# Kernel tuning notes

Hardware: AMD Instinct MI355X
Metric: run time of the kernel (lower is better)

The kernel has to match this reference:

```python
import jax, jax.numpy as jnp
import numpy as np

LN_EPS = 1e-5


def setup_inputs() -> dict:
    key = jax.random.key(0)
    ks = jax.random.split(key, 8)
    N, E, D = 50000, 800000, 128
    x = jax.random.normal(ks[0], (N, D), dtype=jnp.float32)
    edge_index = jax.random.randint(ks[1], (2, E), 0, N, dtype=jnp.int64)
    scale = 0.05
    return {
        "x": x,
        "edge_index": edge_index,
        "W1": jax.random.normal(ks[2], (2 * D, D), dtype=jnp.float32) * scale,
        "b1": jnp.zeros((D,), dtype=jnp.float32),
        "W2": jax.random.normal(ks[3], (D, D), dtype=jnp.float32) * scale,
        "b2": jnp.zeros((D,), dtype=jnp.float32),
        "W3": jax.random.normal(ks[4], (D, D), dtype=jnp.float32) * scale,
        "b3": jnp.zeros((D,), dtype=jnp.float32),
        "W4": jax.random.normal(ks[5], (D, D), dtype=jnp.float32) * scale,
        "b4": jnp.zeros((D,), dtype=jnp.float32),
        "gamma": jnp.ones((D,), dtype=jnp.float32),
        "beta": jnp.zeros((D,), dtype=jnp.float32),
    }


def _layernorm(h, gamma, beta):
    mu = jnp.mean(h, axis=-1, keepdims=True)
    var = jnp.mean(jnp.square(h - mu), axis=-1, keepdims=True)
    return (h - mu) * jax.lax.rsqrt(var + LN_EPS) * gamma + beta


def reference(x, edge_index, W1, b1, W2, b2, W3, b3, W4, b4, gamma, beta):
    num_nodes = x.shape[0]
    senders, receivers = edge_index[0], edge_index[1]
    # gather sender features [E, D], scatter-add to receivers -> [N, D]
    agg = jax.ops.segment_sum(x[senders], receivers, num_segments=num_nodes)
    h = jnp.concatenate([x, agg], axis=-1)  # [N, 2D]
    h = jax.nn.relu(h @ W1 + b1)
    h = jax.nn.relu(h @ W2 + b2)
    h = jax.nn.relu(h @ W3 + b3)
    h = h @ W4 + b4
    return _layernorm(h, gamma, beta)
```

## Files before the change

### kernel.cpp

```cpp
#include <hip/hip_runtime.h>
#include <hip/hip_bf16.h>

typedef short short8 __attribute__((ext_vector_type(8)));
typedef float f32x4 __attribute__((ext_vector_type(4)));

#define LN_EPS 1e-5f
#define NBLK 256

__device__ __forceinline__ unsigned short f2bf(float f) {
    unsigned int u = __builtin_bit_cast(unsigned int, f);
    unsigned int r = (u + 0x7FFFu + ((u >> 16) & 1u)) >> 16;
    return (unsigned short)r;
}
__device__ __forceinline__ float bf_lo(unsigned int v) {
    return __builtin_bit_cast(float, v << 16);
}
__device__ __forceinline__ float bf_hi(unsigned int v) {
    return __builtin_bit_cast(float, v & 0xFFFF0000u);
}

__device__ __forceinline__ bool edges_are_i64(const int* ei) {
    return ((ei[1] | ei[3] | ei[5] | ei[7]) == 0);
}

__device__ __forceinline__ void do_hist(
    const int* __restrict__ ei, int* __restrict__ BBC, int E, int chunk,
    int blk, int t, int* hist)
{
    hist[t] = 0;
    __syncthreads();
    int beg = blk * chunk;
    int end = min(E, beg + chunk);
    if (edges_are_i64(ei)) {
        const long long* e64 = (const long long*)ei;
        for (int e = beg + t; e < end; e += 256)
            atomicAdd(&hist[((int)e64[E + e]) >> 8], 1);
    } else {
        for (int e = beg + t; e < end; e += 256)
            atomicAdd(&hist[ei[E + e] >> 8], 1);
    }
    __syncthreads();
    BBC[t * NBLK + blk] = hist[t];
}

__device__ __forceinline__ void do_prep(
    const float* __restrict__ W1, const float* __restrict__ W2,
    const float* __restrict__ W3, const float* __restrict__ W4,
    unsigned short* __restrict__ wt1, unsigned short* __restrict__ wt2,
    unsigned short* __restrict__ wt3, unsigned short* __restrict__ wt4,
    const float4* __restrict__ x4, uint4* __restrict__ xb4, int total8,
    int idx)
{
    if (idx < 32768) {
        int k = idx >> 7, n = idx & 127;
        wt1[n * 256 + k] = f2bf(W1[idx]);
    } else if (idx < 49152) {
        int j = idx - 32768; int k = j >> 7, n = j & 127;
        wt2[n * 128 + k] = f2bf(W2[j]);
    } else if (idx < 65536) {
        int j = idx - 49152; int k = j >> 7, n = j & 127;
        wt3[n * 128 + k] = f2bf(W3[j]);
    } else if (idx < 81920) {
        int j = idx - 65536; int k = j >> 7, n = j & 127;
        wt4[n * 128 + k] = f2bf(W4[j]);
    } else {
        int i = idx - 81920;
        if (i < total8) {
            float4 a = x4[i * 2], b = x4[i * 2 + 1];
            uint4 o;
            o.x = (unsigned int)f2bf(a.x) | ((unsigned int)f2bf(a.y) << 16);
            o.y = (unsigned int)f2bf(a.z) | ((unsigned int)f2bf(a.w) << 16);
            o.z = (unsigned int)f2bf(b.x) | ((unsigned int)f2bf(b.y) << 16);
            o.w = (unsigned int)f2bf(b.z) | ((unsigned int)f2bf(b.w) << 16);
            xb4[i] = o;
        }
    }
}

__global__ __launch_bounds__(256) void hist_prep_kernel(
    const int* __restrict__ ei, int* __restrict__ BBC, int E, int chunk,
    const float* __restrict__ W1, const float* __restrict__ W2,
    const float* __restrict__ W3, const float* __restrict__ W4,
    unsigned short* __restrict__ wt1, unsigned short* __restrict__ wt2,
    unsigned short* __restrict__ wt3, unsigned short* __restrict__ wt4,
    const float4* __restrict__ x4, uint4* __restrict__ xb4, int total8)
{
    __shared__ int sh[256];
    int t = threadIdx.x;
    if (blockIdx.x < NBLK) {
        do_hist(ei, BBC, E, chunk, blockIdx.x, t, sh);
    } else {
        do_prep(W1, W2, W3, W4, wt1, wt2, wt3, wt4, x4, xb4, total8,
                (blockIdx.x - NBLK) * 256 + t);
    }
}

__global__ __launch_bounds__(256) void xcvt_kernel(
    const float4* __restrict__ x4, uint4* __restrict__ xb4, int total8)
{
    int i = blockIdx.x * 256 + threadIdx.x;
    if (i >= total8) return;
    float4 a = x4[i * 2], b = x4[i * 2 + 1];
    uint4 o;
    o.x = (unsigned int)f2bf(a.x) | ((unsigned int)f2bf(a.y) << 16);
    o.y = (unsigned int)f2bf(a.z) | ((unsigned int)f2bf(a.w) << 16);
    o.z = (unsigned int)f2bf(b.x) | ((unsigned int)f2bf(b.y) << 16);
    o.w = (unsigned int)f2bf(b.z) | ((unsigned int)f2bf(b.w) << 16);
    xb4[i] = o;
}

__global__ __launch_bounds__(256) void bucket_scan1_kernel(
    const int* __restrict__ BBC, int* __restrict__ BBL, int* __restrict__ bucketTotal)
{
    __shared__ int sd[256];
    int t = threadIdx.x, b = blockIdx.x;
    int v = BBC[b * NBLK + t];
    sd[t] = v;
    __syncthreads();
    for (int d = 1; d < 256; d <<= 1) {
        int add = (t >= d) ? sd[t - d] : 0;
        __syncthreads();
        sd[t] += add;
        __syncthreads();
    }
    BBL[b * NBLK + t] = sd[t] - v;
    if (t == 255) bucketTotal[b] = sd[255];
}

__global__ __launch_bounds__(256) void bucket_scan2_kernel(
    const int* __restrict__ bucketTotal, int* __restrict__ bucketBase)
{
    __shared__ int sd[256];
    int t = threadIdx.x;
    int v = bucketTotal[t];
    sd[t] = v;
    __syncthreads();
    for (int d = 1; d < 256; d <<= 1) {
        int add = (t >= d) ? sd[t - d] : 0;
        __syncthreads();
        sd[t] += add;
        __syncthreads();
    }
    bucketBase[t] = sd[t] - v;
    if (t == 255) bucketBase[256] = sd[255];
}

__global__ __launch_bounds__(256) void bucket_scatter_kernel(
    const int* __restrict__ ei, const int* __restrict__ BBL,
    const int* __restrict__ bucketBase, unsigned int* __restrict__ packed,
    int E, int chunk)
{
    __shared__ int cur[256];
    int t = threadIdx.x, blk = blockIdx.x;
    cur[t] = bucketBase[t] + BBL[t * NBLK + blk];
    __syncthreads();
    int beg = blk * chunk;
    int end = min(E, beg + chunk);
    if (edges_are_i64(ei)) {
        const long long* e64 = (const long long*)ei;
        for (int e = beg + t; e < end; e += 256) {
            int s = (int)e64[e], r = (int)e64[E + e];
            int pos = atomicAdd(&cur[r >> 8], 1);
            packed[pos] = (unsigned int)s | ((unsigned int)(r & 255) << 24);
        }
    } else {
        for (int e = beg + t; e < end; e += 256) {
            int s = ei[e], r = ei[E + e];
            int pos = atomicAdd(&cur[r >> 8], 1);
            packed[pos] = (unsigned int)s | ((unsigned int)(r & 255) << 24);
        }
    }
}

__global__ __launch_bounds__(256) void bucket_sort_kernel(
    const unsigned int* __restrict__ packed, const int* __restrict__ bucketBase,
    int* __restrict__ offsets, int* __restrict__ sorted, int N)
{
    __shared__ int hist[256];
    __shared__ int sd[256];
    int t = threadIdx.x, b = blockIdx.x;
    int beg = bucketBase[b], end = bucketBase[b + 1];
    hist[t] = 0;
    __syncthreads();
    for (int i = beg + t; i < end; i += 256)
        atomicAdd(&hist[packed[i] >> 24], 1);
    __syncthreads();
    int v = hist[t];
    sd[t] = v;
    __syncthreads();
    for (int d = 1; d < 256; d <<= 1) {
        int add = (t >= d) ? sd[t - d] : 0;
        __syncthreads();
        sd[t] += add;
        __syncthreads();
    }
    int excl = sd[t] - v;
    int idx = b * 256 + t;
    if (idx <= N) offsets[idx] = beg + excl;
    hist[t] = excl;
    __syncthreads();
    for (int i = beg + t; i < end; i += 256) {
        unsigned int p = packed[i];
        int rl = (int)(p >> 24);
        int pos = beg + atomicAdd(&hist[rl], 1);
        sorted[pos] = (int)(p & 0xFFFFFFu);
    }
}

template<bool BF>
__global__ __launch_bounds__(256) void aggregate_kernel(
    const void* __restrict__ xsrc, const int* __restrict__ offsets,
    const int* __restrict__ sorted, unsigned int* __restrict__ aggb, int N)
{
    int wave = threadIdx.x >> 6, lane = threadIdx.x & 63;
    int r = blockIdx.x * 4 + wave;
    if (r >= N) return;
    int beg = offsets[r], end = offsets[r + 1];
    const unsigned int* xb = (const unsigned int*)xsrc;
    const float2* x2 = (const float2*)xsrc;
    float ax0 = 0, ay0 = 0, ax1 = 0, ay1 = 0;
    float ax2 = 0, ay2 = 0, ax3 = 0, ay3 = 0;
    int i = beg;
    for (; i + 8 <= end; i += 8) {
        int s0 = sorted[i + 0];
        int s1 = sorted[i + 1];
        int s2 = sorted[i + 2];
        int s3 = sorted[i + 3];
        int s4 = sorted[i + 4];
        int s5 = sorted[i + 5];
        int s6 = sorted[i + 6];
        int s7 = sorted[i + 7];
        if constexpr (BF) {
            unsigned int v0 = xb[(size_t)s0 * 64 + lane];
            unsigned int v1 = xb[(size_t)s1 * 64 + lane];
            unsigned int v2 = xb[(size_t)s2 * 64 + lane];
            unsigned int v3 = xb[(size_t)s3 * 64 + lane];
            unsigned int v4 = xb[(size_t)s4 * 64 + lane];
            unsigned int v5 = xb[(size_t)s5 * 64 + lane];
            unsigned int v6 = xb[(size_t)s6 * 64 + lane];
            unsigned int v7 = xb[(size_t)s7 * 64 + lane];
            ax0 += bf_lo(v0); ay0 += bf_hi(v0);
            ax1 += bf_lo(v1); ay1 += bf_hi(v1);
            ax2 += bf_lo(v2); ay2 += bf_hi(v2);
            ax3 += bf_lo(v3); ay3 += bf_hi(v3);
            ax0 += bf_lo(v4); ay0 += bf_hi(v4);
            ax1 += bf_lo(v5); ay1 += bf_hi(v5);
            ax2 += bf_lo(v6); ay2 += bf_hi(v6);
            ax3 += bf_lo(v7); ay3 += bf_hi(v7);
        } else {
            float2 v0 = x2[(size_t)s0 * 64 + lane];
            float2 v1 = x2[(size_t)s1 * 64 + lane];
            float2 v2 = x2[(size_t)s2 * 64 + lane];
            float2 v3 = x2[(size_t)s3 * 64 + lane];
            float2 v4 = x2[(size_t)s4 * 64 + lane];
            float2 v5 = x2[(size_t)s5 * 64 + lane];
            float2 v6 = x2[(size_t)s6 * 64 + lane];
            float2 v7 = x2[(size_t)s7 * 64 + lane];
            ax0 += v0.x; ay0 += v0.y; ax1 += v1.x; ay1 += v1.y;
            ax2 += v2.x; ay2 += v2.y; ax3 += v3.x; ay3 += v3.y;
            ax0 += v4.x; ay0 += v4.y; ax1 += v5.x; ay1 += v5.y;
            ax2 += v6.x; ay2 += v6.y; ax3 += v7.x; ay3 += v7.y;
        }
    }
    for (; i + 4 <= end; i += 4) {
        int s0 = sorted[i + 0];
        int s1 = sorted[i + 1];
        int s2 = sorted[i + 2];
        int s3 = sorted[i + 3];
        if constexpr (BF) {
            unsigned int v0 = xb[(size_t)s0 * 64 + lane];
            unsigned int v1 = xb[(size_t)s1 * 64 + lane];
            unsigned int v2 = xb[(size_t)s2 * 64 + lane];
            unsigned int v3 = xb[(size_t)s3 * 64 + lane];
            ax0 += bf_lo(v0); ay0 += bf_hi(v0);
            ax1 += bf_lo(v1); ay1 += bf_hi(v1);
            ax2 += bf_lo(v2); ay2 += bf_hi(v2);
            ax3 += bf_lo(v3); ay3 += bf_hi(v3);
        } else {
            float2 v0 = x2[(size_t)s0 * 64 + lane];
            float2 v1 = x2[(size_t)s1 * 64 + lane];
            float2 v2 = x2[(size_t)s2 * 64 + lane];
            float2 v3 = x2[(size_t)s3 * 64 + lane];
            ax0 += v0.x; ay0 += v0.y; ax1 += v1.x; ay1 += v1.y;
            ax2 += v2.x; ay2 += v2.y; ax3 += v3.x; ay3 += v3.y;
        }
    }
    for (; i < end; ++i) {
        int s = sorted[i];
        if constexpr (BF) {
            unsigned int v = xb[(size_t)s * 64 + lane];
            ax0 += bf_lo(v); ay0 += bf_hi(v);
        } else {
            float2 v = x2[(size_t)s * 64 + lane];
            ax0 += v.x; ay0 += v.y;
        }
    }
    float sx = (ax0 + ax1) + (ax2 + ax3);
    float sy = (ay0 + ay1) + (ay2 + ay3);
    unsigned int pk = (unsigned int)f2bf(sx) | ((unsigned int)f2bf(sy) << 16);
    aggb[(size_t)r * 128 + lane] = pk;
}

template<int K, int RT, bool RELU>
__device__ __forceinline__ void layer_bf16(
    const unsigned short* Hin, int sin,
    const unsigned short* __restrict__ Wt, const float* __restrict__ bias,
    unsigned short* Hout, int sout, int tid)
{
    int lane = tid & 63;
    int w = tid >> 6;
    int r0 = lane & 15, quad = lane >> 4;
    int col0 = w * 32 + r0;
    int col1 = w * 32 + 16 + r0;
    float bias0 = bias[col0], bias1 = bias[col1];
    f32x4 acc[RT][2];
#pragma unroll
    for (int rt = 0; rt < RT; ++rt) { acc[rt][0] = 0.f; acc[rt][1] = 0.f; }
    const unsigned short* wrow0 = Wt + col0 * K + quad * 8;
    const unsigned short* wrow1 = Wt + col1 * K + quad * 8;
    const unsigned short* arow = Hin + r0 * sin + quad * 8;
#pragma unroll
    for (int ks = 0; ks < K / 32; ++ks) {
        short8 bf0 = *(const short8*)(wrow0 + ks * 32);
        short8 bf1 = *(const short8*)(wrow1 + ks * 32);
#pragma unroll
        for (int rt = 0; rt < RT; ++rt) {
            short8 af = *(const short8*)(arow + rt * 16 * sin + ks * 32);
            acc[rt][0] = __builtin_amdgcn_mfma_f32_16x16x32_bf16(af, bf0, acc[rt][0], 0, 0, 0);
            acc[rt][1] = __builtin_amdgcn_mfma_f32_16x16x32_bf16(af, bf1, acc[rt][1], 0, 0, 0);
        }
    }
#pragma unroll
    for (int rt = 0; rt < RT; ++rt) {
#pragma unroll
        for (int i = 0; i < 4; ++i) {
            int row = rt * 16 + quad * 4 + i;
            float v0 = acc[rt][0][i] + bias0;
            float v1 = acc[rt][1][i] + bias1;
            if (RELU) { v0 = fmaxf(v0, 0.f); v1 = fmaxf(v1, 0.f); }
            Hout[row * sout + col0] = f2bf(v0);
            Hout[row * sout + col1] = f2bf(v1);
        }
    }
}

template<int RT>
__device__ __forceinline__ void layer_f32out(
    const unsigned short* Hin, int sin,
    const unsigned short* __restrict__ Wt, const float* __restrict__ bias,
    float* Hout, int sout, int tid)
{
    constexpr int K = 128;
    int lane = tid & 63;
    int w = tid >> 6;
    int r0 = lane & 15, quad = lane >> 4;
    int col0 = w * 32 + r0;
    int col1 = w * 32 + 16 + r0;
    float bias0 = bias[col0], bias1 = bias[col1];
    f32x4 acc[RT][2];
#pragma unroll
    for (int rt = 0; rt < RT; ++rt) { acc[rt][0] = 0.f; acc[rt][1] = 0.f; }
    const unsigned short* wrow0 = Wt + col0 * K + quad * 8;
    const unsigned short* wrow1 = Wt + col1 * K + quad * 8;
    const unsigned short* arow = Hin + r0 * sin + quad * 8;
#pragma unroll
    for (int ks = 0; ks < K / 32; ++ks) {
        short8 bf0 = *(const short8*)(wrow0 + ks * 32);
        short8 bf1 = *(const short8*)(wrow1 + ks * 32);
#pragma unroll
        for (int rt = 0; rt < RT; ++rt) {
            short8 af = *(const short8*)(arow + rt * 16 * sin + ks * 32);
            acc[rt][0] = __builtin_amdgcn_mfma_f32_16x16x32_bf16(af, bf0, acc[rt][0], 0, 0, 0);
            acc[rt][1] = __builtin_amdgcn_mfma_f32_16x16x32_bf16(af, bf1, acc[rt][1], 0, 0, 0);
        }
    }
#pragma unroll
    for (int rt = 0; rt < RT; ++rt) {
#pragma unroll
        for (int i = 0; i < 4; ++i) {
            int row = rt * 16 + quad * 4 + i;
            Hout[row * sout + col0] = acc[rt][0][i] + bias0;
            Hout[row * sout + col1] = acc[rt][1][i] + bias1;
        }
    }
}

template<bool BF>
__global__ __launch_bounds__(256) void mlp_kernel(
    const void* __restrict__ xsrc, const uint2* aggb,
    const unsigned short* __restrict__ wt1, const unsigned short* __restrict__ wt2,
    const unsigned short* __restrict__ wt3, const unsigned short* __restrict__ wt4,
    const float* __restrict__ b1, const float* __restrict__ b2,
    const float* __restrict__ b3, const float* __restrict__ b4,
    const float* __restrict__ gamma, const float* __restrict__ beta,
    float4* out4, int N)
{
    __shared__ unsigned char smem[16896 + 8704];
    unsigned short* HA = (unsigned short*)smem;
    unsigned short* HB = (unsigned short*)(smem + 16896);
    float* H4 = (float*)smem;

    int tid = threadIdx.x;
    int node0 = blockIdx.x * 32;

#pragma unroll
    for (int j = 0; j < 4; ++j) {
        int idx = tid + j * 256;
        int row = idx >> 5, c4 = idx & 31;
        int node = node0 + row;
        unsigned short* p = HA + row * 264 + c4 * 4;
        if constexpr (BF) {
            uint2 vx = make_uint2(0u, 0u);
            if (node < N) vx = ((const uint2*)xsrc)[(size_t)node * 32 + c4];
            *(uint2*)p = vx;
        } else {
            float4 vx = make_float4(0.f, 0.f, 0.f, 0.f);
            if (node < N) vx = ((const float4*)xsrc)[(size_t)node * 32 + c4];
            p[0] = f2bf(vx.x); p[1] = f2bf(vx.y); p[2] = f2bf(vx.z); p[3] = f2bf(vx.w);
        }
        uint2 va = make_uint2(0u, 0u);
        if (node < N) va = aggb[(size_t)node * 64 + c4];
        *(uint2*)(p + 128) = va;
    }
    __syncthreads();

    layer_bf16<256, 2, true>(HA, 264, wt1, b1, HB, 136, tid);
    __syncthreads();
    layer_bf16<128, 2, true>(HB, 136, wt2, b2, HA, 136, tid);
    __syncthreads();
    layer_bf16<128, 2, true>(HA, 136, wt3, b3, HB, 136, tid);
    __syncthreads();
    layer_f32out<2>(HB, 136, wt4, b4, H4, 132, tid);
    __syncthreads();

    if (tid < 128) {
        int row = tid >> 2;
        int part = tid & 3;
        const float* hr = H4 + row * 132 + part * 32;
        float s = 0.f, s2 = 0.f;
#pragma unroll
        for (int j = 0; j < 8; ++j) {
            float4 v = *(const float4*)(hr + j * 4);
            s  += v.x + v.y + v.z + v.w;
            s2 += v.x * v.x + v.y * v.y + v.z * v.z + v.w * v.w;
        }
        s  += __shfl_xor(s, 1);  s  += __shfl_xor(s, 2);
        s2 += __shfl_xor(s2, 1); s2 += __shfl_xor(s2, 2);
        float mu = s * (1.f / 128.f);
        float var = s2 * (1.f / 128.f) - mu * mu;
        float rstd = rsqrtf(fmaxf(var, 0.f) + LN_EPS);
        int node = node0 + row;
        if (node < N) {
#pragma unroll
            for (int j = 0; j < 8; ++j) {
                int c = part * 32 + j * 4;
                float4 v = *(const float4*)(hr + j * 4);
                float4 o;
                o.x = (v.x - mu) * rstd * gamma[c + 0] + beta[c + 0];
                o.y = (v.y - mu) * rstd * gamma[c + 1] + beta[c + 1];
                o.z = (v.z - mu) * rstd * gamma[c + 2] + beta[c + 2];
                o.w = (v.w - mu) * rstd * gamma[c + 3] + beta[c + 3];
                out4[node * 32 + part * 8 + j] = o;
            }
        }
    }
}

extern "C" void kernel_launch(void* const* d_in, const int* in_sizes, int n_in,
                              void* d_out, int out_size, void* d_ws, size_t ws_size,
                              hipStream_t stream) {
    const float* x     = (const float*)d_in[0];
    const int*   edges = (const int*)d_in[1];
    const float* W1 = (const float*)d_in[2];
    const float* b1 = (const float*)d_in[3];
    const float* W2 = (const float*)d_in[4];
    const float* b2 = (const float*)d_in[5];
    const float* W3 = (const float*)d_in[6];
    const float* b3 = (const float*)d_in[7];
    const float* W4 = (const float*)d_in[8];
    const float* b4 = (const float*)d_in[9];
    const float* gamma = (const float*)d_in[10];
    const float* beta  = (const float*)d_in[11];

    int N = in_sizes[0] / 128;
    int E = in_sizes[1] / 2;

    unsigned int* aggb = (unsigned int*)d_out;

    unsigned char* ws = (unsigned char*)d_ws;
    unsigned short* wt1 = (unsigned short*)ws;
    unsigned short* wt2 = wt1 + 128 * 256;
    unsigned short* wt3 = wt2 + 128 * 128;
    unsigned short* wt4 = wt3 + 128 * 128;
    size_t off = (size_t)(128 * 256 + 3 * 128 * 128) * 2;

    size_t packed_bytes = (size_t)E * 4;
    size_t xb_bytes = (size_t)N * 128 * 2;
    size_t region1 = xb_bytes > packed_bytes ? xb_bytes : packed_bytes;
    size_t tail = (size_t)E * 4
                + (size_t)(N + 1) * 4
                + (size_t)2 * 256 * NBLK * 4
                + 256 * 4
                + 260 * 4;
    int tier;
    if (ws_size >= off + xb_bytes + packed_bytes + tail + 1024) tier = 2;
    else if (ws_size >= off + region1 + tail + 1024)            tier = 1;
    else                                                        tier = 0;

    unsigned char* p = ws + off;
    unsigned short* xb = nullptr;
    unsigned int* packed;
    if (tier == 2) {
        xb = (unsigned short*)p;  p += xb_bytes;
        packed = (unsigned int*)p; p += packed_bytes;
    } else if (tier == 1) {
        packed = (unsigned int*)p;
        xb = (unsigned short*)p;
        p += region1;
    } else {
        packed = (unsigned int*)p; p += packed_bytes;
    }
    int* sorted = (int*)p;      p += (size_t)E * 4;
    int* offsets = (int*)p;     p += (size_t)(N + 1) * 4;
    int* BBC = (int*)p;         p += (size_t)256 * NBLK * 4;
    int* BBL = (int*)p;         p += (size_t)256 * NBLK * 4;
    int* bucketTotal = (int*)p; p += 256 * 4;
    int* bucketBase = (int*)p;

    int chunk = (E + NBLK - 1) / NBLK;

    int total8_now = (tier == 2) ? N * 16 : 0;
    int prep_blocks = (81920 + total8_now + 255) / 256;
    hist_prep_kernel<<<NBLK + prep_blocks, 256, 0, stream>>>(
        edges, BBC, E, chunk,
        W1, W2, W3, W4, wt1, wt2, wt3, wt4,
        (const float4*)x, (uint4*)xb, total8_now);

    bucket_scan1_kernel<<<256, 256, 0, stream>>>(BBC, BBL, bucketTotal);
    bucket_scan2_kernel<<<1, 256, 0, stream>>>(bucketTotal, bucketBase);
    bucket_scatter_kernel<<<NBLK, 256, 0, stream>>>(edges, BBL, bucketBase, packed, E, chunk);
    bucket_sort_kernel<<<256, 256, 0, stream>>>(packed, bucketBase, offsets, sorted, N);

    if (tier == 1) {
        int total8 = N * 16;
        xcvt_kernel<<<(total8 + 255) / 256, 256, 0, stream>>>(
            (const float4*)x, (uint4*)xb, total8);
    }

    int agg_blocks = (N + 3) / 4;
    if (tier >= 1)
        aggregate_kernel<true><<<agg_blocks, 256, 0, stream>>>(
            (const void*)xb, offsets, sorted, aggb, N);
    else
        aggregate_kernel<false><<<agg_blocks, 256, 0, stream>>>(
            (const void*)x, offsets, sorted, aggb, N);

    int mlp_blocks = (N + 31) / 32;
    if (tier >= 1)
        mlp_kernel<true><<<mlp_blocks, 256, 0, stream>>>(
            (const void*)xb, (const uint2*)aggb,
            wt1, wt2, wt3, wt4, b1, b2, b3, b4, gamma, beta,
            (float4*)d_out, N);
    else
        mlp_kernel<false><<<mlp_blocks, 256, 0, stream>>>(
            (const void*)x, (const uint2*)aggb,
            wt1, wt2, wt3, wt4, b1, b2, b3, b4, gamma, beta,
            (float4*)d_out, N);
}
```

Baseline: 203.5 us.

## Fuse CSR build stages into one cooperative kernel with grid syncs

Replaces the five-launch CSR construction (histogram+prep, two scans, scatter, bucket sort) with one cooperative kernel of 256 blocks that separates the phases with grid.sync(). This removes per-launch overhead and the idle gaps between small kernels. In exchange, the prep work (weight transposes and x conversion) now runs on only 256 blocks in a strided loop, where it previously had its own extra blocks, and grid-wide barriers add their own cost. The old multi-kernel path is kept as a fallback when cooperative launch is unsupported.

After: 355.2 us. 1.75x slower.

```diff
diff --git a/kernel.cpp b/kernel.cpp
--- a/kernel.cpp
+++ b/kernel.cpp
@@ -1,5 +1,8 @@
 #include <hip/hip_runtime.h>
 #include <hip/hip_bf16.h>
+#include <hip/hip_cooperative_groups.h>
+
+namespace cg = cooperative_groups;
 
 typedef short short8 __attribute__((ext_vector_type(8)));
 typedef float f32x4 __attribute__((ext_vector_type(4)));
@@ -73,6 +76,111 @@
             o.z = (unsigned int)f2bf(b.x) | ((unsigned int)f2bf(b.y) << 16);
             o.w = (unsigned int)f2bf(b.z) | ((unsigned int)f2bf(b.w) << 16);
             xb4[i] = o;
+        }
+    }
+}
+
+struct CsrArgs {
+    const int* ei; int* BBC; int E; int chunk;
+    const float* W1; const float* W2; const float* W3; const float* W4;
+    unsigned short* wt1; unsigned short* wt2; unsigned short* wt3; unsigned short* wt4;
+    const float4* x4; uint4* xb4; int total8;
+    int* BBL; int* bucketTotal; int* bucketBase;
+    unsigned int* packed; int* offsets; int* sorted; int N;
+};
+
+__global__ __launch_bounds__(256) void csr_coop_kernel(CsrArgs a)
+{
+    cg::grid_group grid = cg::this_grid();
+    __shared__ int sh[256];
+    __shared__ int sd[256];
+    int t = threadIdx.x, b = blockIdx.x;
+
+    do_hist(a.ei, a.BBC, a.E, a.chunk, b, t, sh);
+    int prep_total = 81920 + a.total8;
+    for (int idx = b * 256 + t; idx < prep_total; idx += NBLK * 256)
+        do_prep(a.W1, a.W2, a.W3, a.W4, a.wt1, a.wt2, a.wt3, a.wt4,
+                a.x4, a.xb4, a.total8, idx);
+    grid.sync();
+
+    {
+        int v = a.BBC[b * NBLK + t];
+        sd[t] = v;
+        __syncthreads();
+        for (int d = 1; d < 256; d <<= 1) {
+            int add = (t >= d) ? sd[t - d] : 0;
+            __syncthreads();
+            sd[t] += add;
+            __syncthreads();
+        }
+        a.BBL[b * NBLK + t] = sd[t] - v;
+        if (t == 255) a.bucketTotal[b] = sd[255];
+    }
+    grid.sync();
+
+    if (b == 0) {
+        int v = a.bucketTotal[t];
+        sd[t] = v;
+        __syncthreads();
+        for (int d = 1; d < 256; d <<= 1) {
+            int add = (t >= d) ? sd[t - d] : 0;
+            __syncthreads();
+            sd[t] += add;
+            __syncthreads();
+        }
+        a.bucketBase[t] = sd[t] - v;
+        if (t == 255) a.bucketBase[256] = sd[255];
+    }
+    grid.sync();
+
+    {
+        sh[t] = a.bucketBase[t] + a.BBL[t * NBLK + b];
+        __syncthreads();
+        int beg = b * a.chunk;
+        int end = min(a.E, beg + a.chunk);
+        if (edges_are_i64(a.ei)) {
+            const long long* e64 = (const long long*)a.ei;
+            for (int e = beg + t; e < end; e += 256) {
+                int s = (int)e64[e], r = (int)e64[a.E + e];
+                int pos = atomicAdd(&sh[r >> 8], 1);
+                a.packed[pos] = (unsigned int)s | ((unsigned int)(r & 255) << 24);
+            }
+        } else {
+            for (int e = beg + t; e < end; e += 256) {
+                int s = a.ei[e], r = a.ei[a.E + e];
+                int pos = atomicAdd(&sh[r >> 8], 1);
+                a.packed[pos] = (unsigned int)s | ((unsigned int)(r & 255) << 24);
+            }
+        }
+    }
+    grid.sync();
+
+    {
+        int beg = a.bucketBase[b], end = a.bucketBase[b + 1];
+        sh[t] = 0;
+        __syncthreads();
+        for (int i = beg + t; i < end; i += 256)
+            atomicAdd(&sh[a.packed[i] >> 24], 1);
+        __syncthreads();
+        int v = sh[t];
+        sd[t] = v;
+        __syncthreads();
+        for (int d = 1; d < 256; d <<= 1) {
+            int add = (t >= d) ? sd[t - d] : 0;
+            __syncthreads();
+            sd[t] += add;
+            __syncthreads();
+        }
+        int excl = sd[t] - v;
+        int idx = b * 256 + t;
+        if (idx <= a.N) a.offsets[idx] = beg + excl;
+        sh[t] = excl;
+        __syncthreads();
+        for (int i = beg + t; i < end; i += 256) {
+            unsigned int p = a.packed[i];
+            int rl = (int)(p >> 24);
+            int pos = beg + atomicAdd(&sh[rl], 1);
+            a.sorted[pos] = (int)(p & 0xFFFFFFu);
         }
     }
 }
@@ -529,17 +637,38 @@
 
     int chunk = (E + NBLK - 1) / NBLK;
 
+    static int coop_ok = -1;
+    if (coop_ok < 0) {
+        int dev = 0, v = 0;
+        hipGetDevice(&dev);
+        if (hipDeviceGetAttribute(&v, hipDeviceAttributeCooperativeLaunch, dev) != hipSuccess) v = 0;
+        coop_ok = v ? 1 : 0;
+    }
+
     int total8_now = (tier == 2) ? N * 16 : 0;
-    int prep_blocks = (81920 + total8_now + 255) / 256;
-    hist_prep_kernel<<<NBLK + prep_blocks, 256, 0, stream>>>(
-        edges, BBC, E, chunk,
-        W1, W2, W3, W4, wt1, wt2, wt3, wt4,
-        (const float4*)x, (uint4*)xb, total8_now);
-
-    bucket_scan1_kernel<<<256, 256, 0, stream>>>(BBC, BBL, bucketTotal);
-    bucket_scan2_kernel<<<1, 256, 0, stream>>>(bucketTotal, bucketBase);
-    bucket_scatter_kernel<<<NBLK, 256, 0, stream>>>(edges, BBL, bucketBase, packed, E, chunk);
-    bucket_sort_kernel<<<256, 256, 0, stream>>>(packed, bucketBase, offsets, sorted, N);
+
+    if (coop_ok) {
+        CsrArgs a;
+        a.ei = edges; a.BBC = BBC; a.E = E; a.chunk = chunk;
+        a.W1 = W1; a.W2 = W2; a.W3 = W3; a.W4 = W4;
+        a.wt1 = wt1; a.wt2 = wt2; a.wt3 = wt3; a.wt4 = wt4;
+        a.x4 = (const float4*)x; a.xb4 = (uint4*)xb; a.total8 = total8_now;
+        a.BBL = BBL; a.bucketTotal = bucketTotal; a.bucketBase = bucketBase;
+        a.packed = packed; a.offsets = offsets; a.sorted = sorted; a.N = N;
+        void* kargs[] = { &a };
+        hipLaunchCooperativeKernel((const void*)csr_coop_kernel,
+                                   dim3(NBLK), dim3(256), kargs, 0, stream);
+    } else {
+        int prep_blocks = (81920 + total8_now + 255) / 256;
+        hist_prep_kernel<<<NBLK + prep_blocks, 256, 0, stream>>>(
+            edges, BBC, E, chunk,
+            W1, W2, W3, W4, wt1, wt2, wt3, wt4,
+            (const float4*)x, (uint4*)xb, total8_now);
+        bucket_scan1_kernel<<<256, 256, 0, stream>>>(BBC, BBL, bucketTotal);
+        bucket_scan2_kernel<<<1, 256, 0, stream>>>(bucketTotal, bucketBase);
+        bucket_scatter_kernel<<<NBLK, 256, 0, stream>>>(edges, BBL, bucketBase, packed, E, chunk);
+        bucket_sort_kernel<<<256, 256, 0, stream>>>(packed, bucketBase, offsets, sorted, N);
+    }
 
     if (tier == 1) {
         int total8 = N * 16;
```
